# Performance work log

Hardware: AMD Instinct MI355X
Metric: run time of the kernel (lower is better)

## Reference

```python
import jax, jax.numpy as jnp
import numpy as np

# Sizes
N, T, P, D = 1000, 4, 10, 13          # nodes, point types, edge types (T*(T+1)/2), basis dim per point
F, H, EA, K, E = 128, 128, 16, 64, 20000  # node feat, edge hidden, edge attr/feat, edge op bottleneck, edges
I_NODE = D * (D + 1) // 2             # 91: symmetric ('ij=ji') self-block irreps dim
I_EDGE = D * D                        # 169: generic ('ij') block irreps dim
AVG_NEIGH = 20.0


def setup_inputs() -> dict:
    ks = jax.random.split(jax.random.key(0), 16)
    Fin = H + 2 * F                   # edge-op input: [edge_msg, node_h_i, node_h_j]
    return {
        'node_feats': jax.random.normal(ks[0], (N, F), jnp.float32),
        'node_attrs': jax.random.uniform(ks[1], (N, T), dtype=jnp.float32),
        'edge_feats': jax.random.normal(ks[2], (E, EA), jnp.float32),
        'edge_attrs': jax.random.normal(ks[3], (E, EA), jnp.float32),
        'edge_index': jax.random.randint(ks[4], (2, E), 0, N),
        'node_types': jax.random.randint(ks[5], (N,), 0, T),
        'edge_types': jax.random.randint(ks[6], (E,), 0, P),
        'W_msg': jax.random.normal(ks[7], (F, F), jnp.float32) / np.float32(np.sqrt(F)),
        'W_attr': jax.random.normal(ks[8], (T, F), jnp.float32) / np.float32(np.sqrt(T)),
        'W_em': jax.random.normal(ks[9], (2 * F + 2 * EA, H), jnp.float32) / np.float32(np.sqrt(2 * F + 2 * EA)),
        'W_proj': jax.random.normal(ks[10], (Fin, K), jnp.float32) / np.float32(np.sqrt(Fin)),
        'W_node': jax.random.normal(ks[11], (T, F, I_NODE), jnp.float32) / np.float32(np.sqrt(F)),
        'W_edge': jax.random.normal(ks[12], (P, K, I_EDGE), jnp.float32) / np.float32(np.sqrt(K)),
        'cob_node': jax.random.normal(ks[13], (T, I_NODE, D, D), jnp.float32) / np.float32(D),
        'cob_edge': jax.random.normal(ks[14], (P, I_EDGE, D, D), jnp.float32) / np.float32(D),
    }


def reference(node_feats, node_attrs, edge_feats, edge_attrs, edge_index, node_types,
              edge_types, W_msg, W_attr, W_em, W_proj, W_node, W_edge, cob_node, cob_edge):
    src, dst = edge_index[0], edge_index[1]
    # --- node message passing (NodeMessageBlock, simplified linear-aggregate form) ---
    m = node_feats @ W_msg                                             # [N, F]
    agg = jax.ops.segment_sum(m[src], dst, num_segments=N) \
        + jax.ops.segment_sum(m[dst], src, num_segments=N)             # symmetric edge list: both dirs
    node_h = node_feats + agg / AVG_NEIGH + node_attrs @ W_attr        # [N, F]
    # --- edge messages (EdgeMessageBlock, simplified) ---
    e_in = jnp.concatenate([node_h[src], node_h[dst], edge_feats, edge_attrs], axis=-1)
    edge_msg = jnp.tanh(e_in @ W_em)                                   # [E, H]
    # --- self-interaction blocks: per-type gather -> op -> einsum('ni,ixy->nxy', ., cob) ---
    node_irred = jnp.einsum('nf,nfi->ni', node_h, W_node[node_types])  # [N, I_NODE]
    node_blocks = jnp.einsum('ni,nixy->nxy', node_irred, cob_node[node_types])  # [N, D, D]
    # --- interaction blocks: per-edge-type op + change of basis, transpose-symmetrized ---
    onehot = jax.nn.one_hot(edge_types, P, dtype=node_feats.dtype)     # [E, P] type selector

    def edge_block(a, b):
        h = jnp.concatenate([edge_msg, a, b], axis=-1) @ W_proj        # [E, K]
        irr = jnp.einsum('epi,ep->ei', jnp.einsum('ek,pki->epi', h, W_edge), onehot)  # [E, I_EDGE]
        return jnp.einsum('epxy,ep->exy', jnp.einsum('ei,pixy->epxy', irr, cob_edge), onehot)  # [E, D, D]

    blk_ij = edge_block(node_h[src], node_h[dst])
    blk_ji = edge_block(node_h[dst], node_h[src])
    edge_blocks = 0.5 * (blk_ij + jnp.swapaxes(blk_ji, -1, -2))        # symm_transpose
    # --- scatter blocks into the dense symmetric block matrix ---
    off = jnp.arange(D)
    nidx = jnp.arange(N)[:, None] * D + off                            # [N, D] diagonal block rows/cols
    rs = src[:, None] * D + off                                        # [E, D]
    cs = dst[:, None] * D + off
    M = jnp.zeros((N * D, N * D), node_feats.dtype)
    M = M.at[nidx[:, :, None], nidx[:, None, :]].add(node_blocks)
    M = M.at[rs[:, :, None], cs[:, None, :]].add(edge_blocks)
    M = M.at[cs[:, :, None], rs[:, None, :]].add(jnp.swapaxes(edge_blocks, -1, -2))
    return M
```

## Files before the change

### kernel.cpp

```cpp
#include <hip/hip_runtime.h>
#include <cmath>

#define NN   1000
#define TT   4
#define PP   10
#define DD   13
#define FF   128
#define HH   128
#define EAA  16
#define KDIM 64
#define EE   20000
#define I_NODE 91
#define I_EDGE 169
#define MROW  13000
#define OUT_FLOAT4 42250000L

#define NB_CE   640
#define NB_CN   512
#define NB_MSG  1000
#define NB_ZERO 8192
#define NB_FRONT (NB_CE + NB_CN + NB_MSG + NB_ZERO)

__global__ __launch_bounds__(256) void k_front(
    const float* __restrict__ We, const float* __restrict__ cobE,
    const float* __restrict__ Wn, const float* __restrict__ cobN,
    const float* __restrict__ nf, const float* __restrict__ Wmsg,
    float* __restrict__ Wcomb, float* __restrict__ Wnc,
    float* __restrict__ m, float* __restrict__ agg,
    float4* __restrict__ Mz) {
  int b = blockIdx.x, t = threadIdx.x;
  if (b < NB_CE) {
    if (t < I_EDGE) {
      int pk = b, p = pk >> 6;
      float acc = 0.f;
      const float* wrow = We + pk * I_EDGE;
      const float* crow = cobE + p * I_EDGE * I_EDGE + t;
      for (int i = 0; i < I_EDGE; ++i) acc += wrow[i] * crow[i * I_EDGE];
      Wcomb[pk * I_EDGE + t] = acc;
    }
  } else if (b < NB_CE + NB_CN) {
    if (t < I_EDGE) {
      int tf = b - NB_CE, ty = tf >> 7;
      float acc = 0.f;
      const float* wrow = Wn + tf * I_NODE;
      const float* crow = cobN + ty * I_NODE * I_EDGE + t;
      for (int i = 0; i < I_NODE; ++i) acc += wrow[i] * crow[i * I_EDGE];
      Wnc[tf * I_EDGE + t] = acc;
    }
  } else if (b < NB_CE + NB_CN + NB_MSG) {
    int n = b - (NB_CE + NB_CN);
    __shared__ float row[FF];
    if (t < FF) row[t] = nf[n * FF + t];
    __syncthreads();
    if (t < FF) {
      float acc = 0.f;
#pragma unroll 8
      for (int f = 0; f < FF; ++f) acc += row[f] * Wmsg[f * FF + t];
      m[n * FF + t] = acc;
    } else {
      agg[n * FF + (t - FF)] = 0.f;
    }
  } else {
    long base = (long)(b - (NB_CE + NB_CN + NB_MSG)) * 256 + t;
    const long stride = (long)NB_ZERO * 256;
    float4 z = make_float4(0.f, 0.f, 0.f, 0.f);
    for (long i = base; i < OUT_FLOAT4; i += stride) Mz[i] = z;
  }
}

__global__ __launch_bounds__(256) void k_scatter(
    const float* __restrict__ m, const int* __restrict__ src,
    const int* __restrict__ dst, float* __restrict__ agg) {
  int idx = blockIdx.x * 256 + threadIdx.x;
  if (idx >= EE * FF) return;
  int e = idx >> 7, j = idx & 127;
  int s = src[e], d = dst[e];
  atomicAdd(&agg[d * FF + j], m[s * FF + j]);
  atomicAdd(&agg[s * FF + j], m[d * FF + j]);
}

__global__ __launch_bounds__(192) void k_nodes(
    const float* __restrict__ nf, const float* __restrict__ agg,
    const float* __restrict__ na, const float* __restrict__ Wattr,
    const float* __restrict__ Wem, const float* __restrict__ Wproj,
    const int* __restrict__ ntype, const float* __restrict__ Wnc,
    float* __restrict__ nh, float* __restrict__ V1, float* __restrict__ V2,
    float* __restrict__ U, float* __restrict__ M) {
  int n = blockIdx.x, t = threadIdx.x;
  int ty = ntype[n];
  __shared__ float row[FF];
  if (t < FF) {
    float a = 0.f;
#pragma unroll
    for (int q = 0; q < TT; ++q) a += na[n * TT + q] * Wattr[q * FF + t];
    float v = nf[n * FF + t] + agg[n * FF + t] * (1.0f / 20.0f) + a;
    row[t] = v;
    nh[n * FF + t] = v;
  }
  __syncthreads();
  if (t < FF) {
    float v1 = 0.f, v2 = 0.f;
#pragma unroll 4
    for (int f = 0; f < FF; ++f) {
      float x = row[f];
      v1 += x * Wem[f * HH + t];
      v2 += x * Wem[(FF + f) * HH + t];
    }
    V1[n * HH + t] = v1;
    V2[n * HH + t] = v2;
    int k = t & 63, half = t >> 6;
    const float* W = Wproj + (FF + half * FF) * KDIM + k;
    float u = 0.f;
#pragma unroll 4
    for (int f = 0; f < FF; ++f) u += row[f] * W[f * KDIM];
    U[n * 128 + t] = u;
  }
  if (t < I_EDGE) {
    float acc = 0.f;
    const float* W = Wnc + ty * FF * I_EDGE + t;
#pragma unroll 4
    for (int f = 0; f < FF; ++f) acc += row[f] * W[f * I_EDGE];
    int x = t / DD, y = t % DD;
    atomicAdd(&M[(size_t)(n * DD + x) * MROW + (n * DD + y)], acc);
  }
}

#define EB 4
__global__ __launch_bounds__(768) void k_edge_all(
    const float* __restrict__ V1, const float* __restrict__ V2,
    const float* __restrict__ U, const float* __restrict__ ef,
    const float* __restrict__ ea, const int* __restrict__ src,
    const int* __restrict__ dst, const int* __restrict__ etype,
    const float* __restrict__ Wem, const float* __restrict__ Wproj,
    const float* __restrict__ Wcomb, float* __restrict__ M) {
  int t = threadIdx.x;
  int ei = threadIdx.y;
  int e = blockIdx.x * EB + ei;
  int s = src[e], d = dst[e], p = etype[e];
  __shared__ __align__(16) float efa[EB][32];
  __shared__ __align__(16) float em[EB][HH];
  __shared__ __align__(16) float h[EB][2][KDIM];
  __shared__ __align__(16) float tji[EB][I_EDGE];

  if (t < 32) efa[ei][t] = (t < 16) ? ef[e * EAA + t] : ea[e * EAA + (t - 16)];
  __syncthreads();

  if (t < HH) {
    float acc = V1[s * HH + t] + V2[d * HH + t];
#pragma unroll
    for (int c = 0; c < 32; ++c) acc += efa[ei][c] * Wem[(256 + c) * HH + t];
    em[ei][t] = tanhf(acc);
  }
  __syncthreads();

  if (t < KDIM) {
    float hm = 0.f;
    for (int f = 0; f < HH; f += 4) {
      float4 mv = *(const float4*)&em[ei][f];
      hm += mv.x * Wproj[(f + 0) * KDIM + t] + mv.y * Wproj[(f + 1) * KDIM + t]
          + mv.z * Wproj[(f + 2) * KDIM + t] + mv.w * Wproj[(f + 3) * KDIM + t];
    }
    h[ei][0][t] = hm + U[s * 128 + t] + U[d * 128 + 64 + t];
    h[ei][1][t] = hm + U[d * 128 + t] + U[s * 128 + 64 + t];
  }
  __syncthreads();

  float bij = 0.f, bji = 0.f;
  if (t < I_EDGE) {
    const float* W = Wcomb + p * KDIM * I_EDGE + t;
    for (int k = 0; k < KDIM; k += 4) {
      float4 hi = *(const float4*)&h[ei][0][k];
      float4 hj = *(const float4*)&h[ei][1][k];
      float w0 = W[(k + 0) * I_EDGE], w1 = W[(k + 1) * I_EDGE];
      float w2 = W[(k + 2) * I_EDGE], w3 = W[(k + 3) * I_EDGE];
      bij += hi.x * w0 + hi.y * w1 + hi.z * w2 + hi.w * w3;
      bji += hj.x * w0 + hj.y * w1 + hj.z * w2 + hj.w * w3;
    }
    tji[ei][t] = bji;
  }
  __syncthreads();
  if (t < I_EDGE) {
    int x = t / DD, y = t % DD;
    float eb = 0.5f * (bij + tji[ei][y * DD + x]);
    atomicAdd(&M[(size_t)(s * DD + x) * MROW + (d * DD + y)], eb);
    atomicAdd(&M[(size_t)(d * DD + y) * MROW + (s * DD + x)], eb);
  }
}

extern "C" void kernel_launch(void* const* d_in, const int* in_sizes, int n_in,
                              void* d_out, int out_size, void* d_ws, size_t ws_size,
                              hipStream_t stream) {
  const float* node_feats = (const float*)d_in[0];
  const float* node_attrs = (const float*)d_in[1];
  const float* edge_feats = (const float*)d_in[2];
  const float* edge_attrs = (const float*)d_in[3];
  const int*   edge_index = (const int*)d_in[4];
  const int*   node_types = (const int*)d_in[5];
  const int*   edge_types = (const int*)d_in[6];
  const float* W_msg  = (const float*)d_in[7];
  const float* W_attr = (const float*)d_in[8];
  const float* W_em   = (const float*)d_in[9];
  const float* W_proj = (const float*)d_in[10];
  const float* W_node = (const float*)d_in[11];
  const float* W_edge = (const float*)d_in[12];
  const float* cob_node = (const float*)d_in[13];
  const float* cob_edge = (const float*)d_in[14];

  float* M  = (float*)d_out;
  float* ws = (float*)d_ws;
  float* m_buf = ws;
  float* agg   = ws + 128000;
  float* nh    = ws + 256000;
  float* V1    = ws + 384000;
  float* V2    = ws + 512000;
  float* U     = ws + 640000;
  float* Wcomb = ws + 768000;
  float* Wnc   = ws + 876160;

  const int* src = edge_index;
  const int* dst = edge_index + EE;

  k_front   <<<NB_FRONT, 256, 0, stream>>>(W_edge, cob_edge, W_node, cob_node,
                                           node_feats, W_msg, Wcomb, Wnc,
                                           m_buf, agg, (float4*)M);
  k_scatter <<<(EE * FF) / 256, 256, 0, stream>>>(m_buf, src, dst, agg);
  k_nodes   <<<NN, 192, 0, stream>>>(node_feats, agg, node_attrs, W_attr,
                                     W_em, W_proj, node_types, Wnc,
                                     nh, V1, V2, U, M);
  k_edge_all<<<dim3(EE / EB), dim3(192, 4), 0, stream>>>(V1, V2, U, edge_feats,
                                                         edge_attrs, src, dst,
                                                         edge_types, W_em, W_proj,
                                                         Wcomb, M);
}
```

Measured before the change: 940.3 us.

## Replace atomic scatter into dense matrix with CSR-based per-node block assembly

Edge and node blocks are now written to workspace buffers instead of being atomically added into the huge dense output. A per-node adjacency list is built from degree counts, a prefix scan and atomic cursors. A new assemble kernel then zeroes each node's 13 output rows and adds its diagonal block and all incident edge blocks without atomics. The separate full-matrix zeroing pass in the front kernel goes away. The edge projection is also split across 128 threads with a shared-memory reduction. This adds extra kernels, workspace traffic and a serial per-thread loop over each node's neighbours in assembly.

```diff
diff --git a/kernel.cpp b/kernel.cpp
--- a/kernel.cpp
+++ b/kernel.cpp
@@ -13,21 +13,34 @@
 #define I_NODE 91
 #define I_EDGE 169
 #define MROW  13000
-#define OUT_FLOAT4 42250000L
+#define ROW4  3250
+
+#define WS_EBLK  0L
+#define WS_M     0L
+#define WS_AGG   128000L
+#define WS_NBLK  3380000L
+#define WS_V1    3549000L
+#define WS_V2    3677000L
+#define WS_U     3805000L
+#define WS_WCOMB 3933000L
+#define WS_WNC   4041160L
+#define WS_INT   4127688L
+#define IO_CNT   0
+#define IO_OFF   1000
+#define IO_CUR   2001
+#define IO_ADJ   3001
 
 #define NB_CE   640
 #define NB_CN   512
 #define NB_MSG  1000
-#define NB_ZERO 8192
-#define NB_FRONT (NB_CE + NB_CN + NB_MSG + NB_ZERO)
+#define NB_FRONT (NB_CE + NB_CN + NB_MSG + 1)
 
 __global__ __launch_bounds__(256) void k_front(
     const float* __restrict__ We, const float* __restrict__ cobE,
     const float* __restrict__ Wn, const float* __restrict__ cobN,
     const float* __restrict__ nf, const float* __restrict__ Wmsg,
     float* __restrict__ Wcomb, float* __restrict__ Wnc,
-    float* __restrict__ m, float* __restrict__ agg,
-    float4* __restrict__ Mz) {
+    float* __restrict__ m, float* __restrict__ agg, int* __restrict__ cnt) {
   int b = blockIdx.x, t = threadIdx.x;
   if (b < NB_CE) {
     if (t < I_EDGE) {
@@ -61,20 +74,19 @@
       agg[n * FF + (t - FF)] = 0.f;
     }
   } else {
-    long base = (long)(b - (NB_CE + NB_CN + NB_MSG)) * 256 + t;
-    const long stride = (long)NB_ZERO * 256;
-    float4 z = make_float4(0.f, 0.f, 0.f, 0.f);
-    for (long i = base; i < OUT_FLOAT4; i += stride) Mz[i] = z;
+    for (int i = t; i < NN; i += 256) cnt[i] = 0;
   }
 }
 
 __global__ __launch_bounds__(256) void k_scatter(
     const float* __restrict__ m, const int* __restrict__ src,
-    const int* __restrict__ dst, float* __restrict__ agg) {
+    const int* __restrict__ dst, float* __restrict__ agg,
+    int* __restrict__ cnt) {
   int idx = blockIdx.x * 256 + threadIdx.x;
   if (idx >= EE * FF) return;
   int e = idx >> 7, j = idx & 127;
   int s = src[e], d = dst[e];
+  if (j == 0) { atomicAdd(&cnt[s], 1); atomicAdd(&cnt[d], 1); }
   atomicAdd(&agg[d * FF + j], m[s * FF + j]);
   atomicAdd(&agg[s * FF + j], m[d * FF + j]);
 }
@@ -84,18 +96,41 @@
     const float* __restrict__ na, const float* __restrict__ Wattr,
     const float* __restrict__ Wem, const float* __restrict__ Wproj,
     const int* __restrict__ ntype, const float* __restrict__ Wnc,
-    float* __restrict__ nh, float* __restrict__ V1, float* __restrict__ V2,
-    float* __restrict__ U, float* __restrict__ M) {
-  int n = blockIdx.x, t = threadIdx.x;
+    float* __restrict__ V1, float* __restrict__ V2, float* __restrict__ U,
+    float* __restrict__ nblk, const int* __restrict__ cnt,
+    int* __restrict__ off, int* __restrict__ cur) {
+  int t = threadIdx.x;
+  if (blockIdx.x == NN) {
+    __shared__ int sc[192];
+    int base = t * 6, run = 0, loc[6];
+#pragma unroll
+    for (int i = 0; i < 6; ++i) {
+      int v = (base + i < NN) ? cnt[base + i] : 0;
+      loc[i] = run; run += v;
+    }
+    sc[t] = run;
+    __syncthreads();
+    for (int dd = 1; dd < 192; dd <<= 1) {
+      int v = (t >= dd) ? sc[t - dd] : 0;
+      __syncthreads();
+      sc[t] += v;
+      __syncthreads();
+    }
+    int excl = (t == 0) ? 0 : sc[t - 1];
+#pragma unroll
+    for (int i = 0; i < 6; ++i)
+      if (base + i < NN) { int o = excl + loc[i]; off[base + i] = o; cur[base + i] = o; }
+    if (t == 0) off[NN] = sc[191];
+    return;
+  }
+  int n = blockIdx.x;
   int ty = ntype[n];
   __shared__ float row[FF];
   if (t < FF) {
     float a = 0.f;
 #pragma unroll
     for (int q = 0; q < TT; ++q) a += na[n * TT + q] * Wattr[q * FF + t];
-    float v = nf[n * FF + t] + agg[n * FF + t] * (1.0f / 20.0f) + a;
-    row[t] = v;
-    nh[n * FF + t] = v;
+    row[t] = nf[n * FF + t] + agg[n * FF + t] * (1.0f / 20.0f) + a;
   }
   __syncthreads();
   if (t < FF) {
@@ -120,8 +155,7 @@
     const float* W = Wnc + ty * FF * I_EDGE + t;
 #pragma unroll 4
     for (int f = 0; f < FF; ++f) acc += row[f] * W[f * I_EDGE];
-    int x = t / DD, y = t % DD;
-    atomicAdd(&M[(size_t)(n * DD + x) * MROW + (n * DD + y)], acc);
+    nblk[n * I_EDGE + t] = acc;
   }
 }
 
@@ -132,16 +166,22 @@
     const float* __restrict__ ea, const int* __restrict__ src,
     const int* __restrict__ dst, const int* __restrict__ etype,
     const float* __restrict__ Wem, const float* __restrict__ Wproj,
-    const float* __restrict__ Wcomb, float* __restrict__ M) {
+    const float* __restrict__ Wcomb, float* __restrict__ eblk,
+    int* __restrict__ cur, int* __restrict__ adj) {
   int t = threadIdx.x;
   int ei = threadIdx.y;
   int e = blockIdx.x * EB + ei;
   int s = src[e], d = dst[e], p = etype[e];
   __shared__ __align__(16) float efa[EB][32];
   __shared__ __align__(16) float em[EB][HH];
+  __shared__ __align__(16) float hp[EB][2][KDIM];
   __shared__ __align__(16) float h[EB][2][KDIM];
   __shared__ __align__(16) float tji[EB][I_EDGE];
 
+  if (t == 0) {
+    int pos = atomicAdd(&cur[s], 1); adj[pos] = 2 * e;
+    int pos2 = atomicAdd(&cur[d], 1); adj[pos2] = 2 * e + 1;
+  }
   if (t < 32) efa[ei][t] = (t < 16) ? ef[e * EAA + t] : ea[e * EAA + (t - 16)];
   __syncthreads();
 
@@ -153,13 +193,19 @@
   }
   __syncthreads();
 
+  if (t < 128) {
+    int k = t & 63, half = t >> 6;
+    float hm = 0.f;
+    for (int f = half * 64; f < half * 64 + 64; f += 4) {
+      float4 mv = *(const float4*)&em[ei][f];
+      hm += mv.x * Wproj[(f + 0) * KDIM + k] + mv.y * Wproj[(f + 1) * KDIM + k]
+          + mv.z * Wproj[(f + 2) * KDIM + k] + mv.w * Wproj[(f + 3) * KDIM + k];
+    }
+    hp[ei][half][k] = hm;
+  }
+  __syncthreads();
   if (t < KDIM) {
-    float hm = 0.f;
-    for (int f = 0; f < HH; f += 4) {
-      float4 mv = *(const float4*)&em[ei][f];
-      hm += mv.x * Wproj[(f + 0) * KDIM + t] + mv.y * Wproj[(f + 1) * KDIM + t]
-          + mv.z * Wproj[(f + 2) * KDIM + t] + mv.w * Wproj[(f + 3) * KDIM + t];
-    }
+    float hm = hp[ei][0][t] + hp[ei][1][t];
     h[ei][0][t] = hm + U[s * 128 + t] + U[d * 128 + 64 + t];
     h[ei][1][t] = hm + U[d * 128 + t] + U[s * 128 + 64 + t];
   }
@@ -181,9 +227,37 @@
   __syncthreads();
   if (t < I_EDGE) {
     int x = t / DD, y = t % DD;
-    float eb = 0.5f * (bij + tji[ei][y * DD + x]);
-    atomicAdd(&M[(size_t)(s * DD + x) * MROW + (d * DD + y)], eb);
-    atomicAdd(&M[(size_t)(d * DD + y) * MROW + (s * DD + x)], eb);
+    eblk[(size_t)e * I_EDGE + t] = 0.5f * (bij + tji[ei][y * DD + x]);
+  }
+}
+
+__global__ __launch_bounds__(256) void k_assemble(
+    const float* __restrict__ eblk, const float* __restrict__ nblk,
+    const int* __restrict__ off, const int* __restrict__ adj,
+    const int* __restrict__ src, const int* __restrict__ dst,
+    float* __restrict__ M) {
+  int n = blockIdx.x, t = threadIdx.x;
+  float4* M4 = (float4*)M;
+  const float4 z = make_float4(0.f, 0.f, 0.f, 0.f);
+  for (int i = t; i < DD * ROW4; i += 256) {
+    int r = n * DD + i / ROW4;
+    M4[(size_t)r * ROW4 + (i % ROW4)] = z;
+  }
+  __threadfence_block();
+  __syncthreads();
+  if (t < I_EDGE) {
+    int x = t / DD, y = t % DD;
+    size_t rb = (size_t)(n * DD + x) * MROW;
+    M[rb + n * DD + y] += nblk[n * I_EDGE + t];
+    int o0 = off[n], o1 = off[n + 1];
+    for (int idx = o0; idx < o1; ++idx) {
+      int entry = adj[idx];
+      int e = entry >> 1, dir = entry & 1;
+      int other = dir ? src[e] : dst[e];
+      float v = dir ? eblk[(size_t)e * I_EDGE + y * DD + x]
+                    : eblk[(size_t)e * I_EDGE + t];
+      M[rb + other * DD + y] += v;
+    }
   }
 }
 
@@ -208,27 +282,34 @@
 
   float* M  = (float*)d_out;
   float* ws = (float*)d_ws;
-  float* m_buf = ws;
-  float* agg   = ws + 128000;
-  float* nh    = ws + 256000;
-  float* V1    = ws + 384000;
-  float* V2    = ws + 512000;
-  float* U     = ws + 640000;
-  float* Wcomb = ws + 768000;
-  float* Wnc   = ws + 876160;
+  float* eblk  = ws + WS_EBLK;
+  float* m_buf = ws + WS_M;
+  float* agg   = ws + WS_AGG;
+  float* nblk  = ws + WS_NBLK;
+  float* V1    = ws + WS_V1;
+  float* V2    = ws + WS_V2;
+  float* U     = ws + WS_U;
+  float* Wcomb = ws + WS_WCOMB;
+  float* Wnc   = ws + WS_WNC;
+  int*   iw    = (int*)(ws + WS_INT);
+  int*   cnt   = iw + IO_CNT;
+  int*   off   = iw + IO_OFF;
+  int*   cur   = iw + IO_CUR;
+  int*   adj   = iw + IO_ADJ;
 
   const int* src = edge_index;
   const int* dst = edge_index + EE;
 
   k_front   <<<NB_FRONT, 256, 0, stream>>>(W_edge, cob_edge, W_node, cob_node,
                                            node_feats, W_msg, Wcomb, Wnc,
-                                           m_buf, agg, (float4*)M);
-  k_scatter <<<(EE * FF) / 256, 256, 0, stream>>>(m_buf, src, dst, agg);
-  k_nodes   <<<NN, 192, 0, stream>>>(node_feats, agg, node_attrs, W_attr,
-                                     W_em, W_proj, node_types, Wnc,
-                                     nh, V1, V2, U, M);
+                                           m_buf, agg, cnt);
+  k_scatter <<<(EE * FF) / 256, 256, 0, stream>>>(m_buf, src, dst, agg, cnt);
+  k_nodes   <<<NN + 1, 192, 0, stream>>>(node_feats, agg, node_attrs, W_attr,
+                                         W_em, W_proj, node_types, Wnc,
+                                         V1, V2, U, nblk, cnt, off, cur);
   k_edge_all<<<dim3(EE / EB), dim3(192, 4), 0, stream>>>(V1, V2, U, edge_feats,
                                                          edge_attrs, src, dst,
                                                          edge_types, W_em, W_proj,
-                                                         Wcomb, M);
-}
+                                                         Wcomb, eblk, cur, adj);
+  k_assemble<<<NN, 256, 0, stream>>>(eblk, nblk, off, adj, src, dst, M);
+}
```

Measured after the change: 1.093 ms. 16.3% more time.
